# Kernel optimization log

Hardware: AMD Instinct MI355X
Metric: run time of the kernel (lower is better)

The kernel has to match this reference:

```python
import jax, jax.numpy as jnp
import numpy as np

T, B, DIN, H = 1024, 64, 512, 1024
RESET_ID = 0


def setup_inputs() -> dict:
    key = jax.random.key(0)
    ks = jax.random.split(key, 6)
    std = 1.0 / np.sqrt(H)  # reset_parameters(): uniform(-1/sqrt(output_size), +)
    u = lambda k, shape: jax.random.uniform(k, shape, jnp.float32, -std, std)
    return {
        "x": jax.random.normal(ks[0], (T, B, DIN), jnp.float32),
        "h0": jnp.zeros((B, H), jnp.float32),
        "c0": jnp.zeros((B, H), jnp.float32),
        "Wi": u(ks[1], (4 * H, DIN)),
        "bi": u(ks[2], (4 * H,)),
        "Wh": u(ks[3], (4 * H, H)),
        "bh": u(ks[4], (4 * H,)),
        "input_tokens": jax.random.randint(ks[5], (T, B), 0, 32),
    }


def reference(x, h0, c0, Wi, bi, Wh, bh, input_tokens):
    Tlen = x.shape[0]
    # precompute input-to-hidden as one big GEMM: [T,B,4H]
    xi = jnp.einsum('tbd,gd->tbg', x, Wi) + bi
    # at step t the cell looks at tokens from step t-1, but only when t > 1
    prev_tok = jnp.roll(input_tokens, 1, axis=0)
    do_reset = jnp.broadcast_to((jnp.arange(Tlen) > 1)[:, None], (Tlen, x.shape[1]))

    def step(carry, xs):
        h, c = carry
        xi_t, tok, flag = xs
        keep = jnp.where(flag & (tok == RESET_ID), 0.0, 1.0)[:, None]  # [B,1]
        h = h * keep
        c = c * keep
        preact = xi_t + h @ Wh.T + bh  # [B,4H]
        i = jax.nn.sigmoid(preact[:, :H])
        f = jax.nn.sigmoid(preact[:, H:2 * H])
        o = jax.nn.sigmoid(preact[:, 2 * H:3 * H])
        g = jnp.tanh(preact[:, 3 * H:])  # NOTE: g from last quarter (source quirk)
        c_t = f * c + i * g
        h_t = o * jnp.tanh(c_t)
        return (h_t, c_t), h_t

    (hT, cT), out = jax.lax.scan(step, (h0, c0), (xi, prev_tok, do_reset))
    return out, hT, cT
```

## Files before the change

kernel.cpp:

```cpp
#include <hip/hip_runtime.h>


#define TT   1024
#define BB   64
#define DIN_ 512
#define HH   1024
#define BH   (BB * HH)
#define BD   (BB * DIN_)

typedef __attribute__((ext_vector_type(8))) short  short8;
typedef __attribute__((ext_vector_type(4))) float  floatx4;

__device__ __forceinline__ unsigned short f2bf(float f) {
    unsigned u = __builtin_bit_cast(unsigned, f);
    unsigned r = u + 0x7FFFu + ((u >> 16) & 1u);
    return (unsigned short)(r >> 16);
}
__device__ __forceinline__ float b2f(unsigned short u) {
    return __builtin_bit_cast(float, (unsigned)u << 16);
}
__device__ __forceinline__ short8 frag_f32(const float* __restrict__ p) {
    floatx4 f0 = *(const floatx4*)p;
    floatx4 f1 = *(const floatx4*)(p + 4);
    short8 a;
#pragma unroll
    for (int e = 0; e < 4; ++e) {
        a[e]     = (short)f2bf(f0[e]);
        a[e + 4] = (short)f2bf(f1[e]);
    }
    return a;
}
__device__ __forceinline__ float sigm(float x) { return 1.f / (1.f + __expf(-x)); }
__device__ __forceinline__ float ftanh(float x) {
    float e = __expf(2.f * x);
    return 1.f - 2.f / (e + 1.f);
}

#define WS_FLAG  0
#define WS_BSUM  1024
#define WS_CWS   17408
#define WS_HBUF  279552
#define WS_WHB   541696
#define WS_WIB   8930304
#define WS_XTOP  13124608
#define NEED_COMPACT (13124608ull + 2ull * BD * 2ull)
#define NEED_FULL    (13124608ull + (size_t)TT * BD * 2ull)

__global__ __launch_bounds__(64) void dtype_probe(const unsigned short* __restrict__ wi_raw,
                                                  int* __restrict__ flag) {
    int lane = threadIdx.x;
    int pass = 0;
#pragma unroll
    for (int k = 0; k < 4; ++k) {
        unsigned e = (wi_raw[lane * 4 + k] >> 7) & 0xFF;
        pass += (e >= 0x60 && e <= 0x7B) ? 1 : 0;
    }
    for (int off = 32; off > 0; off >>= 1) pass += __shfl_down(pass, off);
    if (lane == 0) *flag = (pass >= 200) ? 1 : 0;
}

__global__ __launch_bounds__(256) void lstm_init(
    const void* __restrict__ h0, const void* __restrict__ c0,
    const void* __restrict__ bi, const void* __restrict__ bh,
    const void* __restrict__ x,
    const int* __restrict__ flag,
    unsigned short* __restrict__ hbuf0, float* __restrict__ c_ws,
    float* __restrict__ bsum, unsigned short* __restrict__ xpp,
    int stage_x0)
{
    const bool isbf = (*flag != 0);
    int i = blockIdx.x * 256 + threadIdx.x;
    hbuf0[i] = isbf ? ((const unsigned short*)h0)[i] : f2bf(((const float*)h0)[i]);
    c_ws[i]  = isbf ? b2f(((const unsigned short*)c0)[i]) : ((const float*)c0)[i];
    if (i < 4 * HH) {
        float vbi = isbf ? b2f(((const unsigned short*)bi)[i]) : ((const float*)bi)[i];
        float vbh = isbf ? b2f(((const unsigned short*)bh)[i]) : ((const float*)bh)[i];
        bsum[i] = vbi + vbh;
    }
    if (stage_x0 && i < BD / 8) {
        if (isbf) *(short8*)(xpp + (size_t)i * 8) =
                      *(const short8*)((const unsigned short*)x + (size_t)i * 8);
        else      *(short8*)(xpp + (size_t)i * 8) = frag_f32((const float*)x + (size_t)i * 8);
    }
}

__global__ __launch_bounds__(256) void conv_ws(
    const void* __restrict__ Wh, const void* __restrict__ Wi,
    const void* __restrict__ x, const int* __restrict__ flag,
    unsigned short* __restrict__ whb, unsigned short* __restrict__ wib,
    unsigned short* __restrict__ xbf, int do_x)
{
    const bool isbf = (*flag != 0);
    const size_t NWH = (size_t)4 * HH * HH / 8;
    const size_t NWI = (size_t)4 * HH * DIN_ / 8;
    const size_t NX  = do_x ? (size_t)TT * BD / 8 : 0;
    const size_t total = NWH + NWI + NX;
    for (size_t i = (size_t)blockIdx.x * 256 + threadIdx.x; i < total;
         i += (size_t)gridDim.x * 256) {
        const void* src; unsigned short* dst; size_t off;
        if (i < NWH)            { src = Wh; dst = whb; off = i; }
        else if (i < NWH + NWI) { src = Wi; dst = wib; off = i - NWH; }
        else                    { src = x;  dst = xbf; off = i - NWH - NWI; }
        if (isbf) *(short8*)(dst + off * 8) =
                      *(const short8*)((const unsigned short*)src + off * 8);
        else      *(short8*)(dst + off * 8) = frag_f32((const float*)src + off * 8);
    }
}

template<int MODE>
__global__ __launch_bounds__(256) void lstm_step(
    const unsigned short* __restrict__ xb,
    unsigned short* __restrict__ xpp_w,
    const unsigned short* __restrict__ whb,
    const unsigned short* __restrict__ wib,
    const float* __restrict__ bsum,
    const int*  __restrict__ tok,
    unsigned short* __restrict__ hbuf,
    float* __restrict__ c_ws,
    float* __restrict__ out,
    const void* __restrict__ xraw,
    const void* __restrict__ WiRaw,
    const void* __restrict__ WhRaw,
    const int*  __restrict__ flag,
    int t)
{
    const int tid  = threadIdx.x;
    const int wave = tid >> 6;
    const int lane = tid & 63;
    const int jb   = blockIdx.x * 4;

    __shared__ float preact[64][17];

    const int m    = lane & 15;
    const int colq = lane & 15;
    const int quad = lane >> 4;
    const int b_a  = wave * 16 + m;
    const int wrow = (colq >> 2) * HH + jb + (colq & 3);

    floatx4 a0 = {0.f,0.f,0.f,0.f}, a1 = {0.f,0.f,0.f,0.f};
    floatx4 a2 = {0.f,0.f,0.f,0.f}, a3 = {0.f,0.f,0.f,0.f};
    const unsigned short* hsrc = hbuf + (size_t)(t & 1) * BH + b_a * HH + quad * 8;

    if constexpr (MODE < 2) {
        const unsigned short* bp = whb + (size_t)wrow * HH + quad * 8;
#pragma unroll
        for (int ki = 0; ki < 32; ki += 4) {
            a0 = __builtin_amdgcn_mfma_f32_16x16x32_bf16(*(const short8*)(hsrc + (ki+0)*32), *(const short8*)(bp + (ki+0)*32), a0, 0,0,0);
            a1 = __builtin_amdgcn_mfma_f32_16x16x32_bf16(*(const short8*)(hsrc + (ki+1)*32), *(const short8*)(bp + (ki+1)*32), a1, 0,0,0);
            a2 = __builtin_amdgcn_mfma_f32_16x16x32_bf16(*(const short8*)(hsrc + (ki+2)*32), *(const short8*)(bp + (ki+2)*32), a2, 0,0,0);
            a3 = __builtin_amdgcn_mfma_f32_16x16x32_bf16(*(const short8*)(hsrc + (ki+3)*32), *(const short8*)(bp + (ki+3)*32), a3, 0,0,0);
        }
    } else {
        const bool isbf = (*flag != 0);
        if (isbf) {
            const unsigned short* bp = (const unsigned short*)WhRaw + (size_t)wrow * HH + quad * 8;
#pragma unroll
            for (int ki = 0; ki < 32; ki += 2) {
                a0 = __builtin_amdgcn_mfma_f32_16x16x32_bf16(*(const short8*)(hsrc + (ki+0)*32), *(const short8*)(bp + (ki+0)*32), a0, 0,0,0);
                a1 = __builtin_amdgcn_mfma_f32_16x16x32_bf16(*(const short8*)(hsrc + (ki+1)*32), *(const short8*)(bp + (ki+1)*32), a1, 0,0,0);
            }
        } else {
            const float* bp = (const float*)WhRaw + (size_t)wrow * HH + quad * 8;
#pragma unroll
            for (int ki = 0; ki < 32; ki += 2) {
                a0 = __builtin_amdgcn_mfma_f32_16x16x32_bf16(*(const short8*)(hsrc + (ki+0)*32), frag_f32(bp + (ki+0)*32), a0, 0,0,0);
                a1 = __builtin_amdgcn_mfma_f32_16x16x32_bf16(*(const short8*)(hsrc + (ki+1)*32), frag_f32(bp + (ki+1)*32), a1, 0,0,0);
            }
        }
    }
    floatx4 hacc = (a0 + a1) + (a2 + a3);

    if (t > 1) {
#pragma unroll
        for (int r = 0; r < 4; ++r) {
            int bb_ = wave * 16 + quad * 4 + r;
            if (tok[(t - 1) * BB + bb_] == 0) hacc[r] = 0.f;
        }
    }

    floatx4 x0 = {0.f,0.f,0.f,0.f}, x1 = {0.f,0.f,0.f,0.f};
    if constexpr (MODE < 2) {
        const unsigned short* xsrc =
            (MODE == 0 ? xb + (size_t)t * BD : xb + (size_t)(t & 1) * BD)
            + b_a * DIN_ + quad * 8;
        const unsigned short* ip = wib + (size_t)wrow * DIN_ + quad * 8;
#pragma unroll
        for (int ki = 0; ki < 16; ki += 2) {
            x0 = __builtin_amdgcn_mfma_f32_16x16x32_bf16(*(const short8*)(xsrc + (ki+0)*32), *(const short8*)(ip + (ki+0)*32), x0, 0,0,0);
            x1 = __builtin_amdgcn_mfma_f32_16x16x32_bf16(*(const short8*)(xsrc + (ki+1)*32), *(const short8*)(ip + (ki+1)*32), x1, 0,0,0);
        }
    } else {
        const bool isbf = (*flag != 0);
        if (isbf) {
            const unsigned short* ap = (const unsigned short*)xraw + (size_t)t * BD + b_a * DIN_ + quad * 8;
            const unsigned short* bp = (const unsigned short*)WiRaw + (size_t)wrow * DIN_ + quad * 8;
#pragma unroll
            for (int ki = 0; ki < 16; ki += 2) {
                x0 = __builtin_amdgcn_mfma_f32_16x16x32_bf16(*(const short8*)(ap + (ki+0)*32), *(const short8*)(bp + (ki+0)*32), x0, 0,0,0);
                x1 = __builtin_amdgcn_mfma_f32_16x16x32_bf16(*(const short8*)(ap + (ki+1)*32), *(const short8*)(bp + (ki+1)*32), x1, 0,0,0);
            }
        } else {
            const float* ap = (const float*)xraw + (size_t)t * BD + b_a * DIN_ + quad * 8;
            const float* bp = (const float*)WiRaw + (size_t)wrow * DIN_ + quad * 8;
#pragma unroll
            for (int ki = 0; ki < 16; ki += 2) {
                x0 = __builtin_amdgcn_mfma_f32_16x16x32_bf16(frag_f32(ap + (ki+0)*32), frag_f32(bp + (ki+0)*32), x0, 0,0,0);
                x1 = __builtin_amdgcn_mfma_f32_16x16x32_bf16(frag_f32(ap + (ki+1)*32), frag_f32(bp + (ki+1)*32), x1, 0,0,0);
            }
        }
    }
    floatx4 p4 = (hacc + x0) + x1;

#pragma unroll
    for (int r = 0; r < 4; ++r)
        preact[wave * 16 + quad * 4 + r][colq] = p4[r];

    if constexpr (MODE == 1) {
        if (t < TT - 1 && tid < 16) {
            const bool isbf = (*flag != 0);
            size_t ch = (size_t)blockIdx.x * 16 + tid;
            unsigned short* dst = xpp_w + (size_t)((t + 1) & 1) * BD + ch * 8;
            if (isbf) *(short8*)dst =
                *(const short8*)((const unsigned short*)xraw + (size_t)(t + 1) * BD + ch * 8);
            else *(short8*)dst = frag_f32((const float*)xraw + (size_t)(t + 1) * BD + ch * 8);
        }
    }
    __syncthreads();

    const int b  = tid >> 2;
    const int jj = tid & 3;
    const int j  = jb + jj;

    float ig = sigm(preact[b][0 * 4 + jj] + bsum[0 * HH + j]);
    float fg = sigm(preact[b][1 * 4 + jj] + bsum[1 * HH + j]);
    float og = sigm(preact[b][2 * 4 + jj] + bsum[2 * HH + j]);
    float gg = ftanh(preact[b][3 * 4 + jj] + bsum[3 * HH + j]);

    float keep   = (t > 1 && tok[(t - 1) * BB + b] == 0) ? 0.f : 1.f;
    float c_prev = c_ws[b * HH + j] * keep;
    float c_t    = fg * c_prev + ig * gg;
    float h_t    = og * ftanh(c_t);

    out[(size_t)t * BH + b * HH + j] = h_t;
    c_ws[b * HH + j] = c_t;
    hbuf[(size_t)((t + 1) & 1) * BH + b * HH + j] = f2bf(h_t);

    if (t == TT - 1) {
        out[(size_t)TT * BH + b * HH + j]      = h_t;
        out[(size_t)TT * BH + BH + b * HH + j] = c_t;
    }
}

extern "C" void kernel_launch(void* const* d_in, const int* in_sizes, int n_in,
                              void* d_out, int out_size, void* d_ws, size_t ws_size,
                              hipStream_t stream) {
    const void* x  = d_in[0];
    const void* h0 = d_in[1];
    const void* c0 = d_in[2];
    const void* Wi = d_in[3];
    const void* bi = d_in[4];
    const void* Wh = d_in[5];
    const void* bh = d_in[6];
    const int* tok = (const int*)d_in[7];
    float* out = (float*)d_out;

    char* ws = (char*)d_ws;
    int*            flag = (int*)(ws + WS_FLAG);
    float*          bsum = (float*)(ws + WS_BSUM);
    float*          c_ws = (float*)(ws + WS_CWS);
    unsigned short* hbuf = (unsigned short*)(ws + WS_HBUF);
    unsigned short* whb  = (unsigned short*)(ws + WS_WHB);
    unsigned short* wib  = (unsigned short*)(ws + WS_WIB);
    unsigned short* xtop = (unsigned short*)(ws + WS_XTOP);

    const int mode = (ws_size >= NEED_FULL) ? 0 : (ws_size >= NEED_COMPACT) ? 1 : 2;

    dtype_probe<<<1, 64, 0, stream>>>((const unsigned short*)Wi, flag);
    lstm_init<<<256, 256, 0, stream>>>(h0, c0, bi, bh, x, flag, hbuf, c_ws,
                                       bsum, xtop, (mode == 1) ? 1 : 0);
    if (mode < 2)
        conv_ws<<<2048, 256, 0, stream>>>(Wh, Wi, x, flag, whb, wib, xtop,
                                          (mode == 0) ? 1 : 0);

    for (int t = 0; t < TT; ++t) {
        if (mode == 0)
            lstm_step<0><<<256, 256, 0, stream>>>(xtop, xtop, whb, wib, bsum, tok,
                                                  hbuf, c_ws, out, x, Wi, Wh, flag, t);
        else if (mode == 1)
            lstm_step<1><<<256, 256, 0, stream>>>(xtop, xtop, whb, wib, bsum, tok,
                                                  hbuf, c_ws, out, x, Wi, Wh, flag, t);
        else
            lstm_step<2><<<256, 256, 0, stream>>>(nullptr, nullptr, nullptr, nullptr,
                                                  bsum, tok, hbuf, c_ws, out,
                                                  x, Wi, Wh, flag, t);
    }
}
```

Baseline: 15.38 ms.

## Split K across waves and move reset mask to state write-back

Each block now uses 1024 threads and owns 8 hidden units instead of 4. The matmul reduction dimension is split across two wave groups, and the partial sums are combined through a larger shared-memory tile. The grid halves to 128 blocks, which shortens the per-wave MFMA chain and should reduce latency per recurrent step. The token reset mask is now applied when h and c are written for the next step, so the step no longer masks the accumulators, at the cost of an extra shared-memory reduction and fewer blocks.

After: 24.93 ms. 62.1% more time.

```diff
diff --git a/kernel.cpp b/kernel.cpp
--- a/kernel.cpp
+++ b/kernel.cpp
@@ -108,7 +108,7 @@
 }
 
 template<int MODE>
-__global__ __launch_bounds__(256) void lstm_step(
+__global__ __launch_bounds__(1024, 4) void lstm_step(
     const unsigned short* __restrict__ xb,
     unsigned short* __restrict__ xpp_w,
     const unsigned short* __restrict__ whb,
@@ -125,26 +125,30 @@
     int t)
 {
     const int tid  = threadIdx.x;
-    const int wave = tid >> 6;
+    const int w    = tid >> 6;
     const int lane = tid & 63;
-    const int jb   = blockIdx.x * 4;
-
-    __shared__ float preact[64][17];
+    const int jb   = blockIdx.x * 8;
+
+    const int bg = w & 3;
+    const int cg = (w >> 2) & 1;
+    const int kh = w >> 3;
+
+    __shared__ float preact[2][64][33];
 
     const int m    = lane & 15;
     const int colq = lane & 15;
     const int quad = lane >> 4;
-    const int b_a  = wave * 16 + m;
-    const int wrow = (colq >> 2) * HH + jb + (colq & 3);
+    const int b_a  = bg * 16 + m;
+    const int wrow = (colq >> 2) * HH + jb + cg * 4 + (colq & 3);
 
     floatx4 a0 = {0.f,0.f,0.f,0.f}, a1 = {0.f,0.f,0.f,0.f};
     floatx4 a2 = {0.f,0.f,0.f,0.f}, a3 = {0.f,0.f,0.f,0.f};
-    const unsigned short* hsrc = hbuf + (size_t)(t & 1) * BH + b_a * HH + quad * 8;
-
+
+    const unsigned short* hsrc = hbuf + (size_t)(t & 1) * BH + b_a * HH + kh * 512 + quad * 8;
     if constexpr (MODE < 2) {
-        const unsigned short* bp = whb + (size_t)wrow * HH + quad * 8;
-#pragma unroll
-        for (int ki = 0; ki < 32; ki += 4) {
+        const unsigned short* bp = whb + (size_t)wrow * HH + kh * 512 + quad * 8;
+#pragma unroll
+        for (int ki = 0; ki < 16; ki += 4) {
             a0 = __builtin_amdgcn_mfma_f32_16x16x32_bf16(*(const short8*)(hsrc + (ki+0)*32), *(const short8*)(bp + (ki+0)*32), a0, 0,0,0);
             a1 = __builtin_amdgcn_mfma_f32_16x16x32_bf16(*(const short8*)(hsrc + (ki+1)*32), *(const short8*)(bp + (ki+1)*32), a1, 0,0,0);
             a2 = __builtin_amdgcn_mfma_f32_16x16x32_bf16(*(const short8*)(hsrc + (ki+2)*32), *(const short8*)(bp + (ki+2)*32), a2, 0,0,0);
@@ -153,101 +157,102 @@
     } else {
         const bool isbf = (*flag != 0);
         if (isbf) {
-            const unsigned short* bp = (const unsigned short*)WhRaw + (size_t)wrow * HH + quad * 8;
-#pragma unroll
-            for (int ki = 0; ki < 32; ki += 2) {
+            const unsigned short* bp = (const unsigned short*)WhRaw + (size_t)wrow * HH + kh * 512 + quad * 8;
+#pragma unroll
+            for (int ki = 0; ki < 16; ki += 2) {
                 a0 = __builtin_amdgcn_mfma_f32_16x16x32_bf16(*(const short8*)(hsrc + (ki+0)*32), *(const short8*)(bp + (ki+0)*32), a0, 0,0,0);
                 a1 = __builtin_amdgcn_mfma_f32_16x16x32_bf16(*(const short8*)(hsrc + (ki+1)*32), *(const short8*)(bp + (ki+1)*32), a1, 0,0,0);
             }
         } else {
-            const float* bp = (const float*)WhRaw + (size_t)wrow * HH + quad * 8;
-#pragma unroll
-            for (int ki = 0; ki < 32; ki += 2) {
+            const float* bp = (const float*)WhRaw + (size_t)wrow * HH + kh * 512 + quad * 8;
+#pragma unroll
+            for (int ki = 0; ki < 16; ki += 2) {
                 a0 = __builtin_amdgcn_mfma_f32_16x16x32_bf16(*(const short8*)(hsrc + (ki+0)*32), frag_f32(bp + (ki+0)*32), a0, 0,0,0);
                 a1 = __builtin_amdgcn_mfma_f32_16x16x32_bf16(*(const short8*)(hsrc + (ki+1)*32), frag_f32(bp + (ki+1)*32), a1, 0,0,0);
             }
         }
     }
-    floatx4 hacc = (a0 + a1) + (a2 + a3);
-
-    if (t > 1) {
-#pragma unroll
-        for (int r = 0; r < 4; ++r) {
-            int bb_ = wave * 16 + quad * 4 + r;
-            if (tok[(t - 1) * BB + bb_] == 0) hacc[r] = 0.f;
-        }
-    }
-
-    floatx4 x0 = {0.f,0.f,0.f,0.f}, x1 = {0.f,0.f,0.f,0.f};
+
     if constexpr (MODE < 2) {
         const unsigned short* xsrc =
             (MODE == 0 ? xb + (size_t)t * BD : xb + (size_t)(t & 1) * BD)
-            + b_a * DIN_ + quad * 8;
-        const unsigned short* ip = wib + (size_t)wrow * DIN_ + quad * 8;
-#pragma unroll
-        for (int ki = 0; ki < 16; ki += 2) {
-            x0 = __builtin_amdgcn_mfma_f32_16x16x32_bf16(*(const short8*)(xsrc + (ki+0)*32), *(const short8*)(ip + (ki+0)*32), x0, 0,0,0);
-            x1 = __builtin_amdgcn_mfma_f32_16x16x32_bf16(*(const short8*)(xsrc + (ki+1)*32), *(const short8*)(ip + (ki+1)*32), x1, 0,0,0);
+            + b_a * DIN_ + kh * 256 + quad * 8;
+        const unsigned short* ip = wib + (size_t)wrow * DIN_ + kh * 256 + quad * 8;
+#pragma unroll
+        for (int ki = 0; ki < 8; ki += 4) {
+            a0 = __builtin_amdgcn_mfma_f32_16x16x32_bf16(*(const short8*)(xsrc + (ki+0)*32), *(const short8*)(ip + (ki+0)*32), a0, 0,0,0);
+            a1 = __builtin_amdgcn_mfma_f32_16x16x32_bf16(*(const short8*)(xsrc + (ki+1)*32), *(const short8*)(ip + (ki+1)*32), a1, 0,0,0);
+            a2 = __builtin_amdgcn_mfma_f32_16x16x32_bf16(*(const short8*)(xsrc + (ki+2)*32), *(const short8*)(ip + (ki+2)*32), a2, 0,0,0);
+            a3 = __builtin_amdgcn_mfma_f32_16x16x32_bf16(*(const short8*)(xsrc + (ki+3)*32), *(const short8*)(ip + (ki+3)*32), a3, 0,0,0);
         }
     } else {
         const bool isbf = (*flag != 0);
         if (isbf) {
-            const unsigned short* ap = (const unsigned short*)xraw + (size_t)t * BD + b_a * DIN_ + quad * 8;
-            const unsigned short* bp = (const unsigned short*)WiRaw + (size_t)wrow * DIN_ + quad * 8;
-#pragma unroll
-            for (int ki = 0; ki < 16; ki += 2) {
-                x0 = __builtin_amdgcn_mfma_f32_16x16x32_bf16(*(const short8*)(ap + (ki+0)*32), *(const short8*)(bp + (ki+0)*32), x0, 0,0,0);
-                x1 = __builtin_amdgcn_mfma_f32_16x16x32_bf16(*(const short8*)(ap + (ki+1)*32), *(const short8*)(bp + (ki+1)*32), x1, 0,0,0);
+            const unsigned short* ap = (const unsigned short*)xraw + (size_t)t * BD + b_a * DIN_ + kh * 256 + quad * 8;
+            const unsigned short* bp = (const unsigned short*)WiRaw + (size_t)wrow * DIN_ + kh * 256 + quad * 8;
+#pragma unroll
+            for (int ki = 0; ki < 8; ki += 2) {
+                a0 = __builtin_amdgcn_mfma_f32_16x16x32_bf16(*(const short8*)(ap + (ki+0)*32), *(const short8*)(bp + (ki+0)*32), a0, 0,0,0);
+                a1 = __builtin_amdgcn_mfma_f32_16x16x32_bf16(*(const short8*)(ap + (ki+1)*32), *(const short8*)(bp + (ki+1)*32), a1, 0,0,0);
             }
         } else {
-            const float* ap = (const float*)xraw + (size_t)t * BD + b_a * DIN_ + quad * 8;
-            const float* bp = (const float*)WiRaw + (size_t)wrow * DIN_ + quad * 8;
-#pragma unroll
-            for (int ki = 0; ki < 16; ki += 2) {
-                x0 = __builtin_amdgcn_mfma_f32_16x16x32_bf16(frag_f32(ap + (ki+0)*32), frag_f32(bp + (ki+0)*32), x0, 0,0,0);
-                x1 = __builtin_amdgcn_mfma_f32_16x16x32_bf16(frag_f32(ap + (ki+1)*32), frag_f32(bp + (ki+1)*32), x1, 0,0,0);
+            const float* ap = (const float*)xraw + (size_t)t * BD + b_a * DIN_ + kh * 256 + quad * 8;
+            const float* bp = (const float*)WiRaw + (size_t)wrow * DIN_ + kh * 256 + quad * 8;
+#pragma unroll
+            for (int ki = 0; ki < 8; ki += 2) {
+                a0 = __builtin_amdgcn_mfma_f32_16x16x32_bf16(frag_f32(ap + (ki+0)*32), frag_f32(bp + (ki+0)*32), a0, 0,0,0);
+                a1 = __builtin_amdgcn_mfma_f32_16x16x32_bf16(frag_f32(ap + (ki+1)*32), frag_f32(bp + (ki+1)*32), a1, 0,0,0);
             }
         }
     }
-    floatx4 p4 = (hacc + x0) + x1;
-
+
+    floatx4 s = (a0 + a1) + (a2 + a3);
 #pragma unroll
     for (int r = 0; r < 4; ++r)
-        preact[wave * 16 + quad * 4 + r][colq] = p4[r];
-
-    if constexpr (MODE == 1) {
-        if (t < TT - 1 && tid < 16) {
+        preact[kh][bg * 16 + quad * 4 + r][cg * 16 + colq] = s[r];
+    __syncthreads();
+
+    if (tid < 512) {
+        const int b   = tid >> 3;
+        const int jj  = tid & 7;
+        const int j   = jb + jj;
+        const int cge = jj >> 2;
+        const int jc  = jj & 3;
+
+        float p[4];
+#pragma unroll
+        for (int q = 0; q < 4; ++q) {
+            int pc = cge * 16 + q * 4 + jc;
+            p[q] = preact[0][b][pc] + preact[1][b][pc] + bsum[q * HH + j];
+        }
+        float ig = sigm(p[0]);
+        float fg = sigm(p[1]);
+        float og = sigm(p[2]);
+        float gg = ftanh(p[3]);
+
+        float c_prev = c_ws[b * HH + j];
+        float c_t    = fg * c_prev + ig * gg;
+        float h_t    = og * ftanh(c_t);
+
+        out[(size_t)t * BH + b * HH + j] = h_t;
+
+        float kn = (t >= 1 && tok[t * BB + b] == 0) ? 0.f : 1.f;
+        c_ws[b * HH + j] = c_t * kn;
+        hbuf[(size_t)((t + 1) & 1) * BH + b * HH + j] = f2bf(h_t * kn);
+
+        if (t == TT - 1) {
+            out[(size_t)TT * BH + b * HH + j]      = h_t;
+            out[(size_t)TT * BH + BH + b * HH + j] = c_t;
+        }
+    } else if (MODE == 1 && tid < 544) {
+        if (t < TT - 1) {
             const bool isbf = (*flag != 0);
-            size_t ch = (size_t)blockIdx.x * 16 + tid;
+            size_t ch = (size_t)blockIdx.x * 32 + (tid - 512);
             unsigned short* dst = xpp_w + (size_t)((t + 1) & 1) * BD + ch * 8;
             if (isbf) *(short8*)dst =
                 *(const short8*)((const unsigned short*)xraw + (size_t)(t + 1) * BD + ch * 8);
             else *(short8*)dst = frag_f32((const float*)xraw + (size_t)(t + 1) * BD + ch * 8);
         }
-    }
-    __syncthreads();
-
-    const int b  = tid >> 2;
-    const int jj = tid & 3;
-    const int j  = jb + jj;
-
-    float ig = sigm(preact[b][0 * 4 + jj] + bsum[0 * HH + j]);
-    float fg = sigm(preact[b][1 * 4 + jj] + bsum[1 * HH + j]);
-    float og = sigm(preact[b][2 * 4 + jj] + bsum[2 * HH + j]);
-    float gg = ftanh(preact[b][3 * 4 + jj] + bsum[3 * HH + j]);
-
-    float keep   = (t > 1 && tok[(t - 1) * BB + b] == 0) ? 0.f : 1.f;
-    float c_prev = c_ws[b * HH + j] * keep;
-    float c_t    = fg * c_prev + ig * gg;
-    float h_t    = og * ftanh(c_t);
-
-    out[(size_t)t * BH + b * HH + j] = h_t;
-    c_ws[b * HH + j] = c_t;
-    hbuf[(size_t)((t + 1) & 1) * BH + b * HH + j] = f2bf(h_t);
-
-    if (t == TT - 1) {
-        out[(size_t)TT * BH + b * HH + j]      = h_t;
-        out[(size_t)TT * BH + BH + b * HH + j] = c_t;
     }
 }
 
@@ -284,14 +289,14 @@
 
     for (int t = 0; t < TT; ++t) {
         if (mode == 0)
-            lstm_step<0><<<256, 256, 0, stream>>>(xtop, xtop, whb, wib, bsum, tok,
-                                                  hbuf, c_ws, out, x, Wi, Wh, flag, t);
+            lstm_step<0><<<128, 1024, 0, stream>>>(xtop, xtop, whb, wib, bsum, tok,
+                                                   hbuf, c_ws, out, x, Wi, Wh, flag, t);
         else if (mode == 1)
-            lstm_step<1><<<256, 256, 0, stream>>>(xtop, xtop, whb, wib, bsum, tok,
-                                                  hbuf, c_ws, out, x, Wi, Wh, flag, t);
+            lstm_step<1><<<128, 1024, 0, stream>>>(xtop, xtop, whb, wib, bsum, tok,
+                                                   hbuf, c_ws, out, x, Wi, Wh, flag, t);
         else
-            lstm_step<2><<<256, 256, 0, stream>>>(nullptr, nullptr, nullptr, nullptr,
-                                                  bsum, tok, hbuf, c_ws, out,
-                                                  x, Wi, Wh, flag, t);
-    }
-}
+            lstm_step<2><<<128, 1024, 0, stream>>>(nullptr, nullptr, nullptr, nullptr,
+                                                   bsum, tok, hbuf, c_ws, out,
+                                                   x, Wi, Wh, flag, t);
+    }
+}
```
